# Kernel optimization log

Measured on AMD Instinct MI355X. Metric: run time of the kernel, lower is better.

The kernel has to match this reference:

```python
import jax, jax.numpy as jnp
import numpy as np

T, B, H = 1024, 256, 256

def setup_inputs() -> dict:
    key = jax.random.key(0)
    k1, k2, k3, k4 = jax.random.split(key, 4)
    ins = jax.random.normal(k1, (T, B, H), dtype=jnp.float32)
    resets = jax.random.bernoulli(k2, 0.01, (T, B))
    h0 = jnp.zeros((B, H), dtype=jnp.float32)
    s = 1.0 / np.sqrt(H)
    Wi = jax.random.normal(k3, (H, 3 * H), dtype=jnp.float32) * s   # [r|z|n]
    bi = jnp.zeros((3 * H,), dtype=jnp.float32)
    Wh = jax.random.normal(k4, (H, 3 * H), dtype=jnp.float32) * s   # [r|z|n]
    bhn = jnp.zeros((H,), dtype=jnp.float32)
    return {"ins": ins, "resets": resets, "h0": h0,
            "Wi": Wi, "bi": bi, "Wh": Wh, "bhn": bhn}


def reference(ins, resets, h0, Wi, bi, Wh, bhn):
    """GRU scan with reset masking (flax GRUCell semantics).

    ins:    [T, B, H] float inputs (input dim == hidden dim by construction)
    resets: [T, B]    bool, True -> zero the carry before the cell
    returns ys: [T, B, H]
    """
    # Precompute input-side gate projections for all timesteps at once
    # (faithful: same math as per-step dense, just batched over T).
    gi_all = jnp.einsum('tbd,dh->tbh', ins, Wi) + bi  # [T, B, 3H]

    def step(h, xt):
        gi, rst = xt                                   # [B,3H], [B]
        h = jnp.where(rst[:, None], 0.0, h)            # reset masking
        gh = h @ Wh                                    # [B, 3H]
        ir, iz, inn = jnp.split(gi, 3, axis=-1)
        hr, hz, hn = jnp.split(gh, 3, axis=-1)
        r = jax.nn.sigmoid(ir + hr)
        z = jax.nn.sigmoid(iz + hz)
        n = jnp.tanh(inn + r * (hn + bhn))             # flax: hn branch has its own bias
        h_new = (1.0 - z) * n + z * h
        return h_new, h_new                            # GRUCell returns (new_h, new_h)

    _, ys = jax.lax.scan(step, h0, (gi_all, resets))
    return ys
```

## Files before the change

### kernel.cpp

```cpp
#include <hip/hip_runtime.h>
#include <hip/hip_fp16.h>

typedef unsigned int u32;
typedef _Float16 half2v __attribute__((ext_vector_type(2)));
typedef _Float16 half4v __attribute__((ext_vector_type(4)));
typedef _Float16 half8v __attribute__((ext_vector_type(8)));
typedef float f32x4 __attribute__((ext_vector_type(4)));

#define T_DIM 1024
#define B_DIM 256
#define H_DIM 256
#define G_DIM 768

__global__ void prep_kernel(const float* __restrict__ Wi,
                            const float* __restrict__ Wh,
                            _Float16* __restrict__ WiT,
                            _Float16* __restrict__ WhT) {
  int idx = blockIdx.x * 256 + threadIdx.x;
  const int total = G_DIM * H_DIM;
  const float* src = Wi;
  _Float16* dst = WiT;
  if (idx >= total) { idx -= total; src = Wh; dst = WhT; }
  int g = idx >> 8;
  int k = idx & 255;
  dst[idx] = (_Float16)src[(size_t)k * G_DIM + g];
}

#define BM 128
#define BN 128
#define BK 64
#define LDK 72

__global__ __launch_bounds__(256, 2) void gemm_gi_kernel(
    const float* __restrict__ A,
    const _Float16* __restrict__ BT,
    const float* __restrict__ bias,
    _Float16* __restrict__ C)
{
  __shared__ _Float16 As[BM * LDK];
  __shared__ _Float16 Bs[BN * LDK];

  const int tid  = threadIdx.x;
  const int lane = tid & 63;
  const int wid  = tid >> 6;
  const int wr   = wid >> 1;
  const int wc   = wid & 1;

  const int id   = blockIdx.x;
  const int xcd  = id & 7;
  const int slot = id >> 3;
  const int nt   = slot % 6;
  const int mt   = (slot / 6) * 8 + xcd;
  const int m0 = mt * BM;
  const int n0 = nt * BN;

  f32x4 acc[4][4] = {};

  for (int kt = 0; kt < H_DIM; kt += BK) {
#pragma unroll
    for (int i = 0; i < 8; ++i) {
      int c   = tid + i * 256;
      int row = c >> 4;
      int kc  = (c & 15) << 2;
      const float4 v = *(const float4*)(A + (size_t)(m0 + row) * H_DIM + kt + kc);
      half4v h;
      h.x = (_Float16)v.x; h.y = (_Float16)v.y;
      h.z = (_Float16)v.z; h.w = (_Float16)v.w;
      *(half4v*)(&As[row * LDK + kc]) = h;
    }
#pragma unroll
    for (int i = 0; i < 8; ++i) {
      int c   = tid + i * 256;
      int row = c >> 4;
      int kc  = (c & 15) << 2;
      half4v v = *(const half4v*)(BT + (size_t)(n0 + row) * H_DIM + kt + kc);
      *(half4v*)(&Bs[row * LDK + kc]) = v;
    }
    __syncthreads();

#pragma unroll
    for (int kk = 0; kk < 2; ++kk) {
      half8v af[4], bf[4];
#pragma unroll
      for (int m = 0; m < 4; ++m)
        af[m] = *(const half8v*)(&As[(wr*64 + m*16 + (lane & 15)) * LDK + kk*32 + (lane >> 4)*8]);
#pragma unroll
      for (int n = 0; n < 4; ++n)
        bf[n] = *(const half8v*)(&Bs[(wc*64 + n*16 + (lane & 15)) * LDK + kk*32 + (lane >> 4)*8]);
#pragma unroll
      for (int m = 0; m < 4; ++m)
#pragma unroll
        for (int n = 0; n < 4; ++n)
          acc[m][n] = __builtin_amdgcn_mfma_f32_16x16x32_f16(af[m], bf[n], acc[m][n], 0, 0, 0);
    }
    __syncthreads();
  }

#pragma unroll
  for (int n = 0; n < 4; ++n) {
    const int col = n0 + wc*64 + n*16 + (lane & 15);
    const float bv = bias[col];
#pragma unroll
    for (int m = 0; m < 4; ++m) {
#pragma unroll
      for (int q = 0; q < 4; ++q) {
        const int row = m0 + wr*64 + m*16 + (lane >> 4)*4 + q;
        C[(size_t)row * G_DIM + col] = (_Float16)(acc[m][n][q] + bv);
      }
    }
  }
}

__device__ __forceinline__ float dot2f(u32 a, u32 b, float c) {
#if __has_builtin(__builtin_amdgcn_fdot2)
  return __builtin_amdgcn_fdot2(__builtin_bit_cast(half2v, a),
                                __builtin_bit_cast(half2v, b), c, false);
#else
  half2v av = __builtin_bit_cast(half2v, a);
  half2v bv = __builtin_bit_cast(half2v, b);
  return c + (float)av.x * (float)bv.x + (float)av.y * (float)bv.y;
#endif
}

__device__ __forceinline__ float sigmoidf_fast(float x) {
  return __builtin_amdgcn_rcpf(1.f + __expf(-x));
}
__device__ __forceinline__ float tanhf_fast(float x) {
  return 1.f - 2.f * __builtin_amdgcn_rcpf(__expf(2.f * x) + 1.f);
}

__global__ __launch_bounds__(G_DIM, 3) void gru_scan_kernel(
    const _Float16* __restrict__ WhT,
    const _Float16* __restrict__ gi,
    const int* __restrict__ resets,
    const float* __restrict__ h0,
    const float* __restrict__ bhn,
    float* __restrict__ ys)
{
  const int b = blockIdx.x;
  const int j = threadIdx.x;

  __shared__ __align__(16) _Float16 h_lds[H_DIM];
  __shared__ float ex[G_DIM];
  __shared__ float exn[H_DIM];

  u32 w[128];
  {
    const uint4* wp = (const uint4*)(WhT + (size_t)j * H_DIM);
#pragma unroll
    for (int i = 0; i < 32; ++i) {
      uint4 v = wp[i];
      w[4*i+0] = v.x; w[4*i+1] = v.y; w[4*i+2] = v.z; w[4*i+3] = v.w;
    }
  }

  const float bn = (j >= 2*H_DIM) ? bhn[j - 2*H_DIM] : 0.f;

  float hprev = 0.f;
  {
    const int r0 = resets[b];
    if (j < H_DIM) {
      hprev = r0 ? 0.f : h0[(size_t)b * H_DIM + j];
      h_lds[j] = (_Float16)hprev;
    }
  }
  __syncthreads();

  const _Float16* gptr = gi + (size_t)b * G_DIM + j;

  for (int t = 0; t < T_DIM; ++t) {
    const float gij = (float)gptr[(size_t)t * (B_DIM * G_DIM)];
    const int rstn  = (t + 1 < T_DIM) ? resets[(t + 1) * B_DIM + b] : 0;

    float acc = 0.f;
    const uint4* hb = (const uint4*)h_lds;
#pragma unroll
    for (int i = 0; i < 32; ++i) {
      uint4 hv = hb[i];
      acc = dot2f(w[4*i+0], hv.x, acc);
      acc = dot2f(w[4*i+1], hv.y, acc);
      acc = dot2f(w[4*i+2], hv.z, acc);
      acc = dot2f(w[4*i+3], hv.w, acc);
    }

    if (j < 2*H_DIM) {
      ex[j] = acc + gij;
    } else {
      ex[j] = acc + bn;
      exn[j - 2*H_DIM] = gij;
    }
    __syncthreads();

    if (j < H_DIM) {
      const float r = sigmoidf_fast(ex[j]);
      const float z = sigmoidf_fast(ex[j + H_DIM]);
      const float n = tanhf_fast(exn[j] + r * ex[j + 2*H_DIM]);
      const float hn = (1.f - z) * n + z * hprev;
      ys[(size_t)t * (B_DIM * H_DIM) + (size_t)b * H_DIM + j] = hn;
      hprev = rstn ? 0.f : hn;
      h_lds[j] = (_Float16)hprev;
    }
    __syncthreads();
  }
}

__global__ void sentinel_kernel(float* out, int n) {
  int i = blockIdx.x * 256 + threadIdx.x;
  if (i < n) out[i] = 12345.0f;
}

extern "C" void kernel_launch(void* const* d_in, const int* in_sizes, int n_in,
                              void* d_out, int out_size, void* d_ws, size_t ws_size,
                              hipStream_t stream) {
  const float* ins    = (const float*)d_in[0];
  const int*   resets = (const int*)d_in[1];
  const float* h0     = (const float*)d_in[2];
  const float* Wi     = (const float*)d_in[3];
  const float* bi     = (const float*)d_in[4];
  const float* Wh     = (const float*)d_in[5];
  const float* bhn    = (const float*)d_in[6];
  float* ys = (float*)d_out;

  const size_t wbytes  = (size_t)G_DIM * H_DIM * 2;
  const size_t gibytes = (size_t)T_DIM * B_DIM * G_DIM * 2;
  const size_t need = 2 * wbytes + gibytes;
  if (ws_size < need) {
    sentinel_kernel<<<(out_size + 255) / 256, 256, 0, stream>>>(ys, out_size);
    return;
  }

  char* ws = (char*)d_ws;
  _Float16* WiT = (_Float16*)ws;
  _Float16* WhT = (_Float16*)(ws + wbytes);
  _Float16* gi  = (_Float16*)(ws + 2 * wbytes);

  prep_kernel<<<(2 * G_DIM * H_DIM) / 256, 256, 0, stream>>>(Wi, Wh, WiT, WhT);

  const int M = T_DIM * B_DIM;
  const int nblocks = (M / BM) * (G_DIM / BN);
  gemm_gi_kernel<<<nblocks, 256, 0, stream>>>(ins, WiT, bi, gi);

  gru_scan_kernel<<<B_DIM, G_DIM, 0, stream>>>(WhT, gi, resets, h0, bhn, ys);
}
```

Baseline: 2.035 ms.

## Split GRU scan work so each thread pair computes all gates for one hidden unit

The scan kernel now runs 512 threads per batch row. Each adjacent thread pair owns one hidden unit and splits the K dimension in half, computing the r, z and n dot products together and combining the halves with a lane shuffle. This removes the shared-memory gate exchange and one of the two barriers per timestep, and double-buffers h in LDS. Each thread still holds 192 weight registers, and the final gate math is computed redundantly by both threads of the pair.

```diff
diff --git a/kernel.cpp b/kernel.cpp
--- a/kernel.cpp
+++ b/kernel.cpp
@@ -129,7 +129,7 @@
   return 1.f - 2.f * __builtin_amdgcn_rcpf(__expf(2.f * x) + 1.f);
 }
 
-__global__ __launch_bounds__(G_DIM, 3) void gru_scan_kernel(
+__global__ __launch_bounds__(512, 2) void gru_scan_kernel(
     const _Float16* __restrict__ WhT,
     const _Float16* __restrict__ gi,
     const int* __restrict__ resets,
@@ -137,70 +137,91 @@
     const float* __restrict__ bhn,
     float* __restrict__ ys)
 {
-  const int b = blockIdx.x;
-  const int j = threadIdx.x;
-
-  __shared__ __align__(16) _Float16 h_lds[H_DIM];
-  __shared__ float ex[G_DIM];
-  __shared__ float exn[H_DIM];
-
-  u32 w[128];
+  const int b    = blockIdx.x;
+  const int s    = threadIdx.x;
+  const int j    = s >> 1;
+  const int half = s & 1;
+
+  __shared__ __align__(16) _Float16 hbuf[2][H_DIM];
+
+  u32 wR[64], wZ[64], wN[64];
   {
-    const uint4* wp = (const uint4*)(WhT + (size_t)j * H_DIM);
-#pragma unroll
-    for (int i = 0; i < 32; ++i) {
-      uint4 v = wp[i];
-      w[4*i+0] = v.x; w[4*i+1] = v.y; w[4*i+2] = v.z; w[4*i+3] = v.w;
-    }
-  }
-
-  const float bn = (j >= 2*H_DIM) ? bhn[j - 2*H_DIM] : 0.f;
-
-  float hprev = 0.f;
+    const uint4* pR = (const uint4*)(WhT + (size_t)j         * H_DIM + half * 128);
+    const uint4* pZ = (const uint4*)(WhT + (size_t)(j + 256) * H_DIM + half * 128);
+    const uint4* pN = (const uint4*)(WhT + (size_t)(j + 512) * H_DIM + half * 128);
+#pragma unroll
+    for (int i = 0; i < 16; ++i) {
+      uint4 v = pR[i]; wR[4*i]=v.x; wR[4*i+1]=v.y; wR[4*i+2]=v.z; wR[4*i+3]=v.w;
+    }
+#pragma unroll
+    for (int i = 0; i < 16; ++i) {
+      uint4 v = pZ[i]; wZ[4*i]=v.x; wZ[4*i+1]=v.y; wZ[4*i+2]=v.z; wZ[4*i+3]=v.w;
+    }
+#pragma unroll
+    for (int i = 0; i < 16; ++i) {
+      uint4 v = pN[i]; wN[4*i]=v.x; wN[4*i+1]=v.y; wN[4*i+2]=v.z; wN[4*i+3]=v.w;
+    }
+  }
+
+  const float bn = bhn[j];
+
+  float hprev;
   {
     const int r0 = resets[b];
-    if (j < H_DIM) {
-      hprev = r0 ? 0.f : h0[(size_t)b * H_DIM + j];
-      h_lds[j] = (_Float16)hprev;
-    }
+    hprev = r0 ? 0.f : h0[(size_t)b * H_DIM + j];
+    if (half == 0) hbuf[0][j] = (_Float16)hprev;
   }
   __syncthreads();
 
-  const _Float16* gptr = gi + (size_t)b * G_DIM + j;
-
+  const _Float16* gbase = gi + (size_t)b * G_DIM;
+  float* ybase = ys + (size_t)b * H_DIM + j;
+
+  int p = 0;
   for (int t = 0; t < T_DIM; ++t) {
-    const float gij = (float)gptr[(size_t)t * (B_DIM * G_DIM)];
-    const int rstn  = (t + 1 < T_DIM) ? resets[(t + 1) * B_DIM + b] : 0;
-
-    float acc = 0.f;
-    const uint4* hb = (const uint4*)h_lds;
-#pragma unroll
-    for (int i = 0; i < 32; ++i) {
-      uint4 hv = hb[i];
-      acc = dot2f(w[4*i+0], hv.x, acc);
-      acc = dot2f(w[4*i+1], hv.y, acc);
-      acc = dot2f(w[4*i+2], hv.z, acc);
-      acc = dot2f(w[4*i+3], hv.w, acc);
-    }
-
-    if (j < 2*H_DIM) {
-      ex[j] = acc + gij;
+    const _Float16* gp = gbase + (size_t)t * (B_DIM * G_DIM);
+    const float giR = (float)gp[j];
+    const float giZ = (float)gp[j + 256];
+    const float giN = (float)gp[j + 512];
+    const int rstn = (t + 1 < T_DIM) ? resets[(t + 1) * B_DIM + b] : 0;
+
+    float aR = 0.f, aZ = 0.f, aN = 0.f;
+    const uint4* hb = (const uint4*)(&hbuf[p][half * 128]);
+#pragma unroll
+    for (int c = 0; c < 16; ++c) {
+      const uint4 hv = hb[c];
+      aR = dot2f(wR[4*c  ], hv.x, aR);
+      aZ = dot2f(wZ[4*c  ], hv.x, aZ);
+      aN = dot2f(wN[4*c  ], hv.x, aN);
+      aR = dot2f(wR[4*c+1], hv.y, aR);
+      aZ = dot2f(wZ[4*c+1], hv.y, aZ);
+      aN = dot2f(wN[4*c+1], hv.y, aN);
+      aR = dot2f(wR[4*c+2], hv.z, aR);
+      aZ = dot2f(wZ[4*c+2], hv.z, aZ);
+      aN = dot2f(wN[4*c+2], hv.z, aN);
+      aR = dot2f(wR[4*c+3], hv.w, aR);
+      aZ = dot2f(wZ[4*c+3], hv.w, aZ);
+      aN = dot2f(wN[4*c+3], hv.w, aN);
+    }
+
+    aR += __shfl_xor(aR, 1);
+    aZ += __shfl_xor(aZ, 1);
+    aN += __shfl_xor(aN, 1);
+
+    const float r  = sigmoidf_fast(aR + giR);
+    const float z  = sigmoidf_fast(aZ + giZ);
+    const float n  = tanhf_fast(giN + r * (aN + bn));
+    const float hn = (1.f - z) * n + z * hprev;
+
+    const float hnext = rstn ? 0.f : hn;
+    if (half == 0) {
+      hbuf[p ^ 1][j] = (_Float16)hnext;
     } else {
-      ex[j] = acc + bn;
-      exn[j - 2*H_DIM] = gij;
-    }
+      ybase[(size_t)t * (B_DIM * H_DIM)] = hn;
+    }
+    hprev = hnext;
+
     __syncthreads();
-
-    if (j < H_DIM) {
-      const float r = sigmoidf_fast(ex[j]);
-      const float z = sigmoidf_fast(ex[j + H_DIM]);
-      const float n = tanhf_fast(exn[j] + r * ex[j + 2*H_DIM]);
-      const float hn = (1.f - z) * n + z * hprev;
-      ys[(size_t)t * (B_DIM * H_DIM) + (size_t)b * H_DIM + j] = hn;
-      hprev = rstn ? 0.f : hn;
-      h_lds[j] = (_Float16)hprev;
-    }
-    __syncthreads();
+    p ^= 1;
   }
 }
 
@@ -240,5 +261,5 @@
   const int nblocks = (M / BM) * (G_DIM / BN);
   gemm_gi_kernel<<<nblocks, 256, 0, stream>>>(ins, WiT, bi, gi);
 
-  gru_scan_kernel<<<B_DIM, G_DIM, 0, stream>>>(WhT, gi, resets, h0, bhn, ys);
-}
+  gru_scan_kernel<<<B_DIM, 512, 0, stream>>>(WhT, gi, resets, h0, bhn, ys);
+}
```

After: 1.637 ms. 19.6% less time.

## Rewrite GRU scan recurrence with MFMA, register-resident weights and double-buffered hidden state

Applied to the files above, without the earlier changes.

The scan kernel drops the per-thread fdot2 loop over 768 gate rows. Each block now runs 256 threads (4 waves), and every wave keeps its slice of Wh in registers as MFMA B fragments. It computes the recurrent matvec with 16x16x32 MFMAs, where only one of the 16 rows of A is used because the hidden vector is broadcast. Gate math happens directly in registers, which removes the ex/exn LDS round trip and one of the two barriers per step, and the hidden state is double-buffered. The next step's gi values are prefetched during the MFMAs. This needs about 384 VGPRs of weights per thread, and most MFMA output rows are wasted work.

```diff
diff --git a/kernel.cpp b/kernel.cpp
--- a/kernel.cpp
+++ b/kernel.cpp
@@ -111,17 +111,6 @@
   }
 }
 
-__device__ __forceinline__ float dot2f(u32 a, u32 b, float c) {
-#if __has_builtin(__builtin_amdgcn_fdot2)
-  return __builtin_amdgcn_fdot2(__builtin_bit_cast(half2v, a),
-                                __builtin_bit_cast(half2v, b), c, false);
-#else
-  half2v av = __builtin_bit_cast(half2v, a);
-  half2v bv = __builtin_bit_cast(half2v, b);
-  return c + (float)av.x * (float)bv.x + (float)av.y * (float)bv.y;
-#endif
-}
-
 __device__ __forceinline__ float sigmoidf_fast(float x) {
   return __builtin_amdgcn_rcpf(1.f + __expf(-x));
 }
@@ -129,7 +118,7 @@
   return 1.f - 2.f * __builtin_amdgcn_rcpf(__expf(2.f * x) + 1.f);
 }
 
-__global__ __launch_bounds__(G_DIM, 3) void gru_scan_kernel(
+__global__ __launch_bounds__(256, 1) void gru_scan_kernel(
     const _Float16* __restrict__ WhT,
     const _Float16* __restrict__ gi,
     const int* __restrict__ resets,
@@ -137,70 +126,140 @@
     const float* __restrict__ bhn,
     float* __restrict__ ys)
 {
-  const int b = blockIdx.x;
-  const int j = threadIdx.x;
-
-  __shared__ __align__(16) _Float16 h_lds[H_DIM];
-  __shared__ float ex[G_DIM];
-  __shared__ float exn[H_DIM];
-
-  u32 w[128];
-  {
-    const uint4* wp = (const uint4*)(WhT + (size_t)j * H_DIM);
-#pragma unroll
-    for (int i = 0; i < 32; ++i) {
-      uint4 v = wp[i];
-      w[4*i+0] = v.x; w[4*i+1] = v.y; w[4*i+2] = v.z; w[4*i+3] = v.w;
-    }
-  }
-
-  const float bn = (j >= 2*H_DIM) ? bhn[j - 2*H_DIM] : 0.f;
-
-  float hprev = 0.f;
+  const int b   = blockIdx.x;
+  const int tid = threadIdx.x;
+  const int w   = tid >> 6;
+  const int l   = tid & 63;
+  const int lg  = l >> 4;
+  const int lc  = l & 15;
+
+  __shared__ __align__(16) _Float16 hbuf[2][H_DIM];
+
+  half8v wB[3][4][8];
+#pragma unroll
+  for (int g = 0; g < 3; ++g)
+#pragma unroll
+    for (int q = 0; q < 4; ++q) {
+      const _Float16* bp = WhT + (size_t)(256*g + 64*w + 16*q + lc) * H_DIM + 8*lg;
+#pragma unroll
+      for (int s = 0; s < 8; ++s)
+        wB[g][q][s] = *(const half8v*)(bp + 32*s);
+    }
+
+  float bnq[4];
+#pragma unroll
+  for (int q = 0; q < 4; ++q) bnq[q] = bhn[64*w + 16*q + lc];
+
+  float hprev[4];
   {
     const int r0 = resets[b];
-    if (j < H_DIM) {
-      hprev = r0 ? 0.f : h0[(size_t)b * H_DIM + j];
-      h_lds[j] = (_Float16)hprev;
-    }
+    const float* hp = h0 + (size_t)b * H_DIM;
+#pragma unroll
+    for (int q = 0; q < 4; ++q)
+      hprev[q] = r0 ? 0.f : hp[64*w + 16*q + lc];
+    hbuf[0][tid] = (_Float16)(r0 ? 0.f : hp[tid]);
   }
   __syncthreads();
 
-  const _Float16* gptr = gi + (size_t)b * G_DIM + j;
-
+  const _Float16* gbase = gi + (size_t)b * G_DIM;
+  float* yb = ys + (size_t)b * H_DIM;
+
+  float gcur[12];
+#pragma unroll
+  for (int g = 0; g < 3; ++g)
+#pragma unroll
+    for (int q = 0; q < 4; ++q)
+      gcur[g*4+q] = (float)gbase[256*g + 64*w + 16*q + lc];
+
+  const f32x4 zero4 = {0.f, 0.f, 0.f, 0.f};
+
+  int p = 0;
   for (int t = 0; t < T_DIM; ++t) {
-    const float gij = (float)gptr[(size_t)t * (B_DIM * G_DIM)];
-    const int rstn  = (t + 1 < T_DIM) ? resets[(t + 1) * B_DIM + b] : 0;
-
-    float acc = 0.f;
-    const uint4* hb = (const uint4*)h_lds;
-#pragma unroll
-    for (int i = 0; i < 32; ++i) {
-      uint4 hv = hb[i];
-      acc = dot2f(w[4*i+0], hv.x, acc);
-      acc = dot2f(w[4*i+1], hv.y, acc);
-      acc = dot2f(w[4*i+2], hv.z, acc);
-      acc = dot2f(w[4*i+3], hv.w, acc);
-    }
-
-    if (j < 2*H_DIM) {
-      ex[j] = acc + gij;
+    const char* hb = (const char*)(&hbuf[p][0]);
+
+    half8v a0 = *(const half8v*)(hb +       16*lg);
+    half8v a1 = *(const half8v*)(hb +  64 + 16*lg);
+    half8v a2 = *(const half8v*)(hb + 128 + 16*lg);
+    half8v a3 = *(const half8v*)(hb + 192 + 16*lg);
+
+    f32x4 acc[3][4];
+#pragma unroll
+    for (int g = 0; g < 3; ++g)
+#pragma unroll
+      for (int q = 0; q < 4; ++q)
+        acc[g][q] = __builtin_amdgcn_mfma_f32_16x16x32_f16(a0, wB[g][q][0], zero4, 0, 0, 0);
+#pragma unroll
+    for (int g = 0; g < 3; ++g)
+#pragma unroll
+      for (int q = 0; q < 4; ++q)
+        acc[g][q] = __builtin_amdgcn_mfma_f32_16x16x32_f16(a1, wB[g][q][1], acc[g][q], 0, 0, 0);
+#pragma unroll
+    for (int g = 0; g < 3; ++g)
+#pragma unroll
+      for (int q = 0; q < 4; ++q)
+        acc[g][q] = __builtin_amdgcn_mfma_f32_16x16x32_f16(a2, wB[g][q][2], acc[g][q], 0, 0, 0);
+#pragma unroll
+    for (int g = 0; g < 3; ++g)
+#pragma unroll
+      for (int q = 0; q < 4; ++q)
+        acc[g][q] = __builtin_amdgcn_mfma_f32_16x16x32_f16(a3, wB[g][q][3], acc[g][q], 0, 0, 0);
+
+    half8v a4 = *(const half8v*)(hb + 256 + 16*lg);
+    half8v a5 = *(const half8v*)(hb + 320 + 16*lg);
+    half8v a6 = *(const half8v*)(hb + 384 + 16*lg);
+    half8v a7 = *(const half8v*)(hb + 448 + 16*lg);
+
+    const int rstn = (t + 1 < T_DIM) ? resets[(t + 1) * B_DIM + b] : 0;
+    float gnxt[12];
+    if (t + 1 < T_DIM) {
+      const _Float16* gp = gbase + (size_t)(t + 1) * (B_DIM * G_DIM);
+#pragma unroll
+      for (int g = 0; g < 3; ++g)
+#pragma unroll
+        for (int q = 0; q < 4; ++q)
+          gnxt[g*4+q] = (float)gp[256*g + 64*w + 16*q + lc];
     } else {
-      ex[j] = acc + bn;
-      exn[j - 2*H_DIM] = gij;
-    }
+#pragma unroll
+      for (int i = 0; i < 12; ++i) gnxt[i] = 0.f;
+    }
+
+#pragma unroll
+    for (int g = 0; g < 3; ++g)
+#pragma unroll
+      for (int q = 0; q < 4; ++q)
+        acc[g][q] = __builtin_amdgcn_mfma_f32_16x16x32_f16(a4, wB[g][q][4], acc[g][q], 0, 0, 0);
+#pragma unroll
+    for (int g = 0; g < 3; ++g)
+#pragma unroll
+      for (int q = 0; q < 4; ++q)
+        acc[g][q] = __builtin_amdgcn_mfma_f32_16x16x32_f16(a5, wB[g][q][5], acc[g][q], 0, 0, 0);
+#pragma unroll
+    for (int g = 0; g < 3; ++g)
+#pragma unroll
+      for (int q = 0; q < 4; ++q)
+        acc[g][q] = __builtin_amdgcn_mfma_f32_16x16x32_f16(a6, wB[g][q][6], acc[g][q], 0, 0, 0);
+#pragma unroll
+    for (int g = 0; g < 3; ++g)
+#pragma unroll
+      for (int q = 0; q < 4; ++q)
+        acc[g][q] = __builtin_amdgcn_mfma_f32_16x16x32_f16(a7, wB[g][q][7], acc[g][q], 0, 0, 0);
+
+#pragma unroll
+    for (int q = 0; q < 4; ++q) {
+      const float r  = sigmoidf_fast(acc[0][q][0] + gcur[q]);
+      const float z  = sigmoidf_fast(acc[1][q][0] + gcur[4+q]);
+      const float n  = tanhf_fast(gcur[8+q] + r * (acc[2][q][0] + bnq[q]));
+      const float hn = (1.f - z) * n + z * hprev[q];
+      const float hx = rstn ? 0.f : hn;
+      if (lg == 0) yb[(size_t)t * (B_DIM * H_DIM) + 64*w + 16*q + lc] = hn;
+      if (lg == 1) hbuf[p ^ 1][64*w + 16*q + lc] = (_Float16)hx;
+      hprev[q] = hx;
+    }
+#pragma unroll
+    for (int i = 0; i < 12; ++i) gcur[i] = gnxt[i];
+
     __syncthreads();
-
-    if (j < H_DIM) {
-      const float r = sigmoidf_fast(ex[j]);
-      const float z = sigmoidf_fast(ex[j + H_DIM]);
-      const float n = tanhf_fast(exn[j] + r * ex[j + 2*H_DIM]);
-      const float hn = (1.f - z) * n + z * hprev;
-      ys[(size_t)t * (B_DIM * H_DIM) + (size_t)b * H_DIM + j] = hn;
-      hprev = rstn ? 0.f : hn;
-      h_lds[j] = (_Float16)hprev;
-    }
-    __syncthreads();
+    p ^= 1;
   }
 }
 
@@ -240,5 +299,5 @@
   const int nblocks = (M / BM) * (G_DIM / BN);
   gemm_gi_kernel<<<nblocks, 256, 0, stream>>>(ins, WiT, bi, gi);
 
-  gru_scan_kernel<<<B_DIM, G_DIM, 0, stream>>>(WhT, gi, resets, h0, bhn, ys);
-}
+  gru_scan_kernel<<<B_DIM, 256, 0, stream>>>(WhT, gi, resets, h0, bhn, ys);
+}
```

Result: slower. 2.587 ms (+27.1%).

## Rewrite GRU scan recurrence with MFMA, register-resident weights and double-buffered hidden state

Applied to the files above, without the earlier changes.

The per-step h@Wh product in the scan kernel now runs on MFMA 16x16x32 f16 instructions with the hidden vector broadcast as the A operand, instead of per-thread fdot2 chains. The block shrinks from 768 to 256 threads, and each wave keeps its Wh slice in registers as MFMA B fragments. The gate math is fused into the same threads, so only one barrier per step remains, and h is double-buffered in LDS. The next step's gi values are prefetched. Only row 0 of each MFMA output is used, so 15/16 of the matrix work is wasted, and holding 96 half8 registers per thread limits occupancy to one block per CU.

```diff
diff --git a/kernel.cpp b/kernel.cpp
--- a/kernel.cpp
+++ b/kernel.cpp
@@ -111,17 +111,6 @@
   }
 }
 
-__device__ __forceinline__ float dot2f(u32 a, u32 b, float c) {
-#if __has_builtin(__builtin_amdgcn_fdot2)
-  return __builtin_amdgcn_fdot2(__builtin_bit_cast(half2v, a),
-                                __builtin_bit_cast(half2v, b), c, false);
-#else
-  half2v av = __builtin_bit_cast(half2v, a);
-  half2v bv = __builtin_bit_cast(half2v, b);
-  return c + (float)av.x * (float)bv.x + (float)av.y * (float)bv.y;
-#endif
-}
-
 __device__ __forceinline__ float sigmoidf_fast(float x) {
   return __builtin_amdgcn_rcpf(1.f + __expf(-x));
 }
@@ -129,7 +118,21 @@
   return 1.f - 2.f * __builtin_amdgcn_rcpf(__expf(2.f * x) + 1.f);
 }
 
-__global__ __launch_bounds__(G_DIM, 3) void gru_scan_kernel(
+#define MFMA_GROUP0(AREG)                                                    \
+  _Pragma("unroll")                                                          \
+  for (int g = 0; g < 3; ++g)                                                \
+    _Pragma("unroll")                                                        \
+    for (int q = 0; q < 4; ++q)                                              \
+      acc[g][q] = __builtin_amdgcn_mfma_f32_16x16x32_f16(AREG, wB[g][q][0], zero4, 0, 0, 0);
+
+#define MFMA_GROUP(S, AREG)                                                  \
+  _Pragma("unroll")                                                          \
+  for (int g = 0; g < 3; ++g)                                                \
+    _Pragma("unroll")                                                        \
+    for (int q = 0; q < 4; ++q)                                              \
+      acc[g][q] = __builtin_amdgcn_mfma_f32_16x16x32_f16(AREG, wB[g][q][S], acc[g][q], 0, 0, 0);
+
+__global__ __launch_bounds__(256, 1) void gru_scan_kernel(
     const _Float16* __restrict__ WhT,
     const _Float16* __restrict__ gi,
     const int* __restrict__ resets,
@@ -137,70 +140,108 @@
     const float* __restrict__ bhn,
     float* __restrict__ ys)
 {
-  const int b = blockIdx.x;
-  const int j = threadIdx.x;
-
-  __shared__ __align__(16) _Float16 h_lds[H_DIM];
-  __shared__ float ex[G_DIM];
-  __shared__ float exn[H_DIM];
-
-  u32 w[128];
-  {
-    const uint4* wp = (const uint4*)(WhT + (size_t)j * H_DIM);
-#pragma unroll
-    for (int i = 0; i < 32; ++i) {
-      uint4 v = wp[i];
-      w[4*i+0] = v.x; w[4*i+1] = v.y; w[4*i+2] = v.z; w[4*i+3] = v.w;
-    }
-  }
-
-  const float bn = (j >= 2*H_DIM) ? bhn[j - 2*H_DIM] : 0.f;
-
-  float hprev = 0.f;
+  const int b   = blockIdx.x;
+  const int tid = threadIdx.x;
+  const int w   = tid >> 6;
+  const int l   = tid & 63;
+  const int lg  = l >> 4;
+  const int lc  = l & 15;
+  const int c0  = 64*w + 4*lc;
+
+  __shared__ __align__(16) _Float16 hbuf[2][H_DIM];
+
+  half8v wB[3][4][8];
+#pragma unroll
+  for (int g = 0; g < 3; ++g)
+#pragma unroll
+    for (int q = 0; q < 4; ++q) {
+      const _Float16* bp = WhT + (size_t)(256*g + c0 + q) * H_DIM + 8*lg;
+#pragma unroll
+      for (int s = 0; s < 8; ++s)
+        wB[g][q][s] = *(const half8v*)(bp + 32*s);
+    }
+
+  const float4 bn4 = *(const float4*)(bhn + c0);
+
+  float hprev[4];
   {
     const int r0 = resets[b];
-    if (j < H_DIM) {
-      hprev = r0 ? 0.f : h0[(size_t)b * H_DIM + j];
-      h_lds[j] = (_Float16)hprev;
+    const float4 h4 = *(const float4*)(h0 + (size_t)b * H_DIM + c0);
+    hprev[0] = r0 ? 0.f : h4.x;
+    hprev[1] = r0 ? 0.f : h4.y;
+    hprev[2] = r0 ? 0.f : h4.z;
+    hprev[3] = r0 ? 0.f : h4.w;
+    if (lg == 0) {
+      half4v pk;
+      pk[0] = (_Float16)hprev[0]; pk[1] = (_Float16)hprev[1];
+      pk[2] = (_Float16)hprev[2]; pk[3] = (_Float16)hprev[3];
+      *(half4v*)(&hbuf[0][c0]) = pk;
     }
   }
   __syncthreads();
 
-  const _Float16* gptr = gi + (size_t)b * G_DIM + j;
-
+  const _Float16* gbase = gi + (size_t)b * G_DIM;
+  float* yb = ys + (size_t)b * H_DIM;
+
+  half4v gR = *(const half4v*)(gbase + c0);
+  half4v gZ = *(const half4v*)(gbase + 256 + c0);
+  half4v gN = *(const half4v*)(gbase + 512 + c0);
+
+  const f32x4 zero4 = {0.f, 0.f, 0.f, 0.f};
+
+  int p = 0;
   for (int t = 0; t < T_DIM; ++t) {
-    const float gij = (float)gptr[(size_t)t * (B_DIM * G_DIM)];
-    const int rstn  = (t + 1 < T_DIM) ? resets[(t + 1) * B_DIM + b] : 0;
-
-    float acc = 0.f;
-    const uint4* hb = (const uint4*)h_lds;
-#pragma unroll
-    for (int i = 0; i < 32; ++i) {
-      uint4 hv = hb[i];
-      acc = dot2f(w[4*i+0], hv.x, acc);
-      acc = dot2f(w[4*i+1], hv.y, acc);
-      acc = dot2f(w[4*i+2], hv.z, acc);
-      acc = dot2f(w[4*i+3], hv.w, acc);
-    }
-
-    if (j < 2*H_DIM) {
-      ex[j] = acc + gij;
-    } else {
-      ex[j] = acc + bn;
-      exn[j - 2*H_DIM] = gij;
-    }
+    const int tn = (t + 1 < T_DIM) ? (t + 1) : (T_DIM - 1);
+    const _Float16* gp = gbase + (size_t)tn * (B_DIM * G_DIM);
+    const half4v gRn = *(const half4v*)(gp + c0);
+    const half4v gZn = *(const half4v*)(gp + 256 + c0);
+    const half4v gNn = *(const half4v*)(gp + 512 + c0);
+    const int rstn = (t + 1 < T_DIM) ? resets[tn * B_DIM + b] : 0;
+
+    const char* hb = (const char*)(&hbuf[p][0]);
+    f32x4 acc[3][4];
+    half8v x0 = *(const half8v*)(hb +       16*lg);
+    half8v x1 = *(const half8v*)(hb +  64 + 16*lg);
+    half8v x2 = *(const half8v*)(hb + 128 + 16*lg);
+    MFMA_GROUP0(x0);
+    half8v x3 = *(const half8v*)(hb + 192 + 16*lg);
+    MFMA_GROUP(1, x1);
+    half8v x4 = *(const half8v*)(hb + 256 + 16*lg);
+    MFMA_GROUP(2, x2);
+    half8v x5 = *(const half8v*)(hb + 320 + 16*lg);
+    MFMA_GROUP(3, x3);
+    half8v x6 = *(const half8v*)(hb + 384 + 16*lg);
+    MFMA_GROUP(4, x4);
+    half8v x7 = *(const half8v*)(hb + 448 + 16*lg);
+    MFMA_GROUP(5, x5);
+    MFMA_GROUP(6, x6);
+    MFMA_GROUP(7, x7);
+
+    float hnv[4];
+    half4v pk;
+#pragma unroll
+    for (int q = 0; q < 4; ++q) {
+      const float r  = sigmoidf_fast(acc[0][q][0] + (float)gR[q]);
+      const float z  = sigmoidf_fast(acc[1][q][0] + (float)gZ[q]);
+      const float bq = (q == 0) ? bn4.x : (q == 1) ? bn4.y : (q == 2) ? bn4.z : bn4.w;
+      const float n  = tanhf_fast((float)gN[q] + r * (acc[2][q][0] + bq));
+      const float hn = (1.f - z) * n + z * hprev[q];
+      const float hx = rstn ? 0.f : hn;
+      hnv[q] = hn;
+      pk[q] = (_Float16)hx;
+      hprev[q] = hx;
+    }
+    if (lg == 0) {
+      float4 o; o.x = hnv[0]; o.y = hnv[1]; o.z = hnv[2]; o.w = hnv[3];
+      *(float4*)(yb + (size_t)t * (B_DIM * H_DIM) + c0) = o;
+    }
+    if (lg == 1) {
+      *(half4v*)(&hbuf[p ^ 1][c0]) = pk;
+    }
+    gR = gRn; gZ = gZn; gN = gNn;
+
     __syncthreads();
-
-    if (j < H_DIM) {
-      const float r = sigmoidf_fast(ex[j]);
-      const float z = sigmoidf_fast(ex[j + H_DIM]);
-      const float n = tanhf_fast(exn[j] + r * ex[j + 2*H_DIM]);
-      const float hn = (1.f - z) * n + z * hprev;
-      ys[(size_t)t * (B_DIM * H_DIM) + (size_t)b * H_DIM + j] = hn;
-      hprev = rstn ? 0.f : hn;
-      h_lds[j] = (_Float16)hprev;
-    }
-    __syncthreads();
+    p ^= 1;
   }
 }
 
@@ -240,5 +281,5 @@
   const int nblocks = (M / BM) * (G_DIM / BN);
   gemm_gi_kernel<<<nblocks, 256, 0, stream>>>(ins, WiT, bi, gi);
 
-  gru_scan_kernel<<<B_DIM, G_DIM, 0, stream>>>(WhT, gi, resets, h0, bhn, ys);
-}
+  gru_scan_kernel<<<B_DIM, 256, 0, stream>>>(WhT, gi, resets, h0, bhn, ys);
+}
```

Result: slower. 2.318 ms (+13.9%).
